# Kernel tuning notes

Measured on AMD Instinct MI355X. Metric: run time of the kernel, lower is better.

Reference implementation:

```python
import jax, jax.numpy as jnp
import numpy as np

N = 50000      # total nodes across batch of graphs
E = 800000     # total directed edges (avg degree 16)
B = 64         # number of graphs
D = 128        # input_dim == hidden_dim
L = 4          # num_layers - 1 GIN layers
OUT = 10
BN_EPS = 1e-5


def setup_inputs() -> dict:
    key = jax.random.key(0)
    ks = jax.random.split(key, 12)
    s = 0.05
    return {
        "x": jax.random.normal(ks[0], (N, D), jnp.float32),
        "pi": jax.random.uniform(ks[1], (B, 25), jnp.float32),
        "eps": jnp.zeros((L,), jnp.float32),
        "mlp_w1": jax.random.normal(ks[2], (L, D, D), jnp.float32) * s,
        "mlp_b1": jnp.zeros((L, D), jnp.float32),
        "mlp_bn_g": jnp.ones((L, D), jnp.float32),
        "mlp_bn_b": jnp.zeros((L, D), jnp.float32),
        "mlp_w2": jax.random.normal(ks[3], (L, D, D), jnp.float32) * s,
        "mlp_b2": jnp.zeros((L, D), jnp.float32),
        "bn_g": jnp.ones((L, D), jnp.float32),
        "bn_b": jnp.zeros((L, D), jnp.float32),
        "attend_w": jax.random.normal(ks[4], (D * (L + 1), 1), jnp.float32) * s,
        "attend_b": jnp.zeros((1,), jnp.float32),
        "pi_w": jax.random.normal(ks[5], (25, 16), jnp.float32) * s,
        "pi_b": jnp.zeros((16,), jnp.float32),
        "out_w": jax.random.normal(ks[6], (D * (L + 1) + 16, OUT), jnp.float32) * s,
        "out_b": jnp.zeros((OUT,), jnp.float32),
        "edge_index": jax.random.randint(ks[7], (2, E), 0, N, dtype=jnp.int32),
        "graph_id": jnp.sort(jax.random.randint(ks[8], (N,), 0, B, dtype=jnp.int32)),
    }


def _bn(z, g, b):
    # BatchNorm1d in training mode over all nodes (axis 0)
    m = z.mean(axis=0)
    v = z.var(axis=0)
    return (z - m) * jax.lax.rsqrt(v + BN_EPS) * g + b


def reference(x, pi, eps, mlp_w1, mlp_b1, mlp_bn_g, mlp_bn_b, mlp_w2, mlp_b2,
              bn_g, bn_b, attend_w, attend_b, pi_w, pi_b, out_w, out_b,
              edge_index, graph_id):
    src, dst = edge_index[0], edge_index[1]
    h = x
    reps = [x]
    for l in range(L):
        # GIN sum aggregation (learn_eps=True: no self-loops in Adj)
        pooled = jax.ops.segment_sum(h[src], dst, num_segments=N)
        pooled = pooled + (1.0 + eps[l]) * h
        # 2-layer MLP: Linear -> BN -> ReLU -> Linear
        z = jax.nn.relu(_bn(pooled @ mlp_w1[l] + mlp_b1[l], mlp_bn_g[l], mlp_bn_b[l]))
        z = z @ mlp_w2[l] + mlp_b2[l]
        # outer BN + ReLU
        h = jax.nn.relu(_bn(z, bn_g[l], bn_b[l]))
        reps.append(h)
    hr = jnp.concatenate(reps, axis=1)               # [N, D*(L+1)]
    # per-graph attention softmax over nodes
    scores = (hr @ attend_w + attend_b)[:, 0]        # [N]
    smax = jax.ops.segment_max(scores, graph_id, num_segments=B)
    e = jnp.exp(scores - smax[graph_id])
    denom = jax.ops.segment_sum(e, graph_id, num_segments=B)
    coef = e / denom[graph_id]
    gemb = jax.ops.segment_sum(hr * coef[:, None], graph_id, num_segments=B)  # [B, D*(L+1)]
    # persistence-image branch (PI computed host-side; treated as input)
    pie = jax.nn.relu(pi @ pi_w + pi_b)              # [B, 16]
    feat = jnp.concatenate([gemb, pie], axis=1)      # [B, D*(L+1)+16]
    return feat @ out_w + out_b                      # [B, OUT]
```

## Files before the change

### kernel.cpp

```cpp
#include <hip/hip_runtime.h>
#include <hip/hip_bf16.h>

#define NN 50000
#define EE 800000
#define BBG 64
#define DD 128
#define LLAY 4
#define HRW 640
#define NOUT 10
#define SCANB 196

typedef __hip_bfloat16 bf16;
typedef __attribute__((ext_vector_type(8))) short short8;
typedef __attribute__((ext_vector_type(4))) float f32x4;

__device__ __forceinline__ float b2f(bf16 v) { return __bfloat162float(v); }
__device__ __forceinline__ float bflo(unsigned u) { return __uint_as_float(u << 16); }
__device__ __forceinline__ float bfhi(unsigned u) { return __uint_as_float(u & 0xffff0000u); }
__device__ __forceinline__ unsigned short f2bs(float v) {
  bf16 h = __float2bfloat16(v);
  unsigned short r; __builtin_memcpy(&r, &h, 2); return r;
}
__device__ __forceinline__ int dtype_of(const void* __restrict__ bng) {
  return (*(const unsigned*)bng == 0x3F800000u) ? 1 : 0;
}
__device__ __forceinline__ float ldf(const void* __restrict__ p, long i, int dt) {
  return dt ? ((const float*)p)[i] : b2f(((const bf16*)p)[i]);
}

__device__ __forceinline__ int lower_bound_i(const int* __restrict__ a, int n, int key) {
  int lo = 0, hi = n;
  while (lo < hi) { int mid = (lo + hi) >> 1; if (a[mid] < key) lo = mid + 1; else hi = mid; }
  return lo;
}

__global__ __launch_bounds__(256) void gnn_init(const void* __restrict__ x,
                                                bf16* __restrict__ hrb,
                                                const void* __restrict__ w1,
                                                const void* __restrict__ w2,
                                                bf16* __restrict__ w1t,
                                                bf16* __restrict__ w2t,
                                                const void* __restrict__ aw,
                                                float* __restrict__ scores,
                                                const int* __restrict__ ei,
                                                int* __restrict__ counts,
                                                int* __restrict__ rel,
                                                const void* __restrict__ bng) {
  int dt = dtype_of(bng);
  int tid = threadIdx.x;
  if (blockIdx.x >= 6250) {
    int i = (blockIdx.x - 6250) * 256 + tid;
    int l = i >> 14, rem = i & 16383, n = rem >> 7, k = rem & 127;
    long src = (long)l * 16384 + k * 128 + n;
    w1t[i] = __float2bfloat16(ldf(w1, src, dt));
    w2t[i] = __float2bfloat16(ldf(w2, src, dt));
    return;
  }
  if (blockIdx.x >= 3125) {
    int e = (blockIdx.x - 3125) * 256 + tid;
    rel[e] = atomicAdd(&counts[ei[EE + e]], 1);
    return;
  }
  int n = blockIdx.x * 16 + (tid >> 4);
  int il = tid & 15;
  long base = (long)n * DD + il * 8;
  float v[8];
  if (dt) {
    float4 a0 = *(const float4*)((const float*)x + base);
    float4 a1 = *(const float4*)((const float*)x + base + 4);
    v[0] = a0.x; v[1] = a0.y; v[2] = a0.z; v[3] = a0.w;
    v[4] = a1.x; v[5] = a1.y; v[6] = a1.z; v[7] = a1.w;
  } else {
    uint4 u = *(const uint4*)((const bf16*)x + base);
    v[0] = bflo(u.x); v[1] = bfhi(u.x); v[2] = bflo(u.y); v[3] = bfhi(u.y);
    v[4] = bflo(u.z); v[5] = bfhi(u.z); v[6] = bflo(u.w); v[7] = bfhi(u.w);
  }
  uint4 o;
  o.x = (unsigned)f2bs(v[0]) | ((unsigned)f2bs(v[1]) << 16);
  o.y = (unsigned)f2bs(v[2]) | ((unsigned)f2bs(v[3]) << 16);
  o.z = (unsigned)f2bs(v[4]) | ((unsigned)f2bs(v[5]) << 16);
  o.w = (unsigned)f2bs(v[6]) | ((unsigned)f2bs(v[7]) << 16);
  *(uint4*)(hrb + (size_t)n * HRW + il * 8) = o;
  float ss = 0.f;
  #pragma unroll
  for (int k = 0; k < 8; k++) ss += v[k] * ldf(aw, il * 8 + k, dt);
  ss += __shfl_xor(ss, 1, 64); ss += __shfl_xor(ss, 2, 64);
  ss += __shfl_xor(ss, 4, 64); ss += __shfl_xor(ss, 8, 64);
  if (il == 0) unsafeAtomicAdd(&scores[n], ss);
}

__global__ __launch_bounds__(256) void gnn_scan1(const int* __restrict__ counts,
                                                 int* __restrict__ blocksum) {
  __shared__ int buf[256];
  int tid = threadIdx.x;
  int i = blockIdx.x * 256 + tid;
  buf[tid] = (i < NN) ? counts[i] : 0;
  __syncthreads();
  for (int s = 128; s > 0; s >>= 1) {
    if (tid < s) buf[tid] += buf[tid + s];
    __syncthreads();
  }
  if (tid == 0) blocksum[blockIdx.x] = buf[0];
}

__global__ __launch_bounds__(256) void gnn_scan3(const int* __restrict__ counts,
                                                 const int* __restrict__ blocksum,
                                                 int* __restrict__ rowstart) {
  __shared__ int buf[256];
  int tid = threadIdx.x;
  int partial = 0;
  for (int i = tid; i < blockIdx.x; i += 256) partial += blocksum[i];
  buf[tid] = partial;
  __syncthreads();
  for (int s = 128; s > 0; s >>= 1) {
    if (tid < s) buf[tid] += buf[tid + s];
    __syncthreads();
  }
  int offset = buf[0];
  __syncthreads();
  int i = blockIdx.x * 256 + tid;
  int v = (i < NN) ? counts[i] : 0;
  buf[tid] = v;
  __syncthreads();
  for (int ofs = 1; ofs < 256; ofs <<= 1) {
    int t = (tid >= ofs) ? buf[tid - ofs] : 0;
    __syncthreads();
    buf[tid] += t;
    __syncthreads();
  }
  int val = offset + buf[tid] - v;
  if (i < NN) rowstart[i] = val;
  if (blockIdx.x == SCANB - 1 && tid == 255) rowstart[NN] = offset + buf[255];
}

__global__ __launch_bounds__(256) void gnn_fill(const int* __restrict__ ei,
                                                const int* __restrict__ rowstart,
                                                const int* __restrict__ rel,
                                                int* __restrict__ csr_src) {
  int e = blockIdx.x * 256 + threadIdx.x;
  int src = ei[e];
  int dst = ei[EE + e];
  csr_src[rowstart[dst] + rel[e]] = src;
}

__device__ __forceinline__ void acc8(float* a, uint4 u) {
  a[0] += bflo(u.x); a[1] += bfhi(u.x);
  a[2] += bflo(u.y); a[3] += bfhi(u.y);
  a[4] += bflo(u.z); a[5] += bfhi(u.z);
  a[6] += bflo(u.w); a[7] += bfhi(u.w);
}

__device__ __forceinline__ float2 statsum(const float* __restrict__ stat, int c) {
  float s = 0.f, q = 0.f;
  #pragma unroll
  for (int k = 0; k < 8; k++) { s += stat[k * 256 + c]; q += stat[k * 256 + 128 + c]; }
  return make_float2(s, q);
}

__global__ __launch_bounds__(512) void gnn_gmg1(const bf16* __restrict__ hrb, int l,
                                                const int* __restrict__ rowstart,
                                                const int* __restrict__ csr_src,
                                                const void* __restrict__ eps,
                                                const bf16* __restrict__ Wt,
                                                const void* __restrict__ bias, int biasOfs,
                                                bf16* __restrict__ out,
                                                float* __restrict__ statOut,
                                                const void* __restrict__ bng) {
  int dt = dtype_of(bng);
  __shared__ __align__(16) unsigned ar[16][68];
  __shared__ int qhead;
  int tid = threadIdx.x, lane = tid & 63;
  int w = tid >> 6;
  int q = lane >> 4, il = lane & 15;
  int r0 = blockIdx.x * 16;
  const bf16* stripe = hrb + l * DD;
  float s = 1.0f + ldf(eps, l, dt);
  if (tid == 0) qhead = 0;
  __syncthreads();

  for (;;) {
    int i;
    if (lane == 0) i = atomicAdd(&qhead, 1);
    i = __shfl(i, 0, 64);
    if (i >= 16) break;
    int n = r0 + i;
    float a[8] = {0.f, 0.f, 0.f, 0.f, 0.f, 0.f, 0.f, 0.f};
    if (q == 0) {
      uint4 u = *(const uint4*)(stripe + (size_t)n * HRW + il * 8);
      a[0] = s * bflo(u.x); a[1] = s * bfhi(u.x);
      a[2] = s * bflo(u.y); a[3] = s * bfhi(u.y);
      a[4] = s * bflo(u.z); a[5] = s * bfhi(u.z);
      a[6] = s * bflo(u.w); a[7] = s * bfhi(u.w);
    }
    int start = rowstart[n], end = rowstart[n + 1];
    for (int base = start; base < end; base += 64) {
      int m = end - base; if (m > 64) m = 64;
      int idx = (base + lane < end) ? csr_src[base + lane] : 0;
      int j = 0;
      for (; j + 16 <= m; j += 16) {
        int s0 = __shfl(idx, j + q, 64);
        int s1 = __shfl(idx, j + 4 + q, 64);
        int s2 = __shfl(idx, j + 8 + q, 64);
        int s3 = __shfl(idx, j + 12 + q, 64);
        uint4 u0 = *(const uint4*)(stripe + (size_t)s0 * HRW + il * 8);
        uint4 u1 = *(const uint4*)(stripe + (size_t)s1 * HRW + il * 8);
        uint4 u2 = *(const uint4*)(stripe + (size_t)s2 * HRW + il * 8);
        uint4 u3 = *(const uint4*)(stripe + (size_t)s3 * HRW + il * 8);
        acc8(a, u0); acc8(a, u1); acc8(a, u2); acc8(a, u3);
      }
      for (; j + 8 <= m; j += 8) {
        int s0 = __shfl(idx, j + q, 64);
        int s1 = __shfl(idx, j + 4 + q, 64);
        uint4 u0 = *(const uint4*)(stripe + (size_t)s0 * HRW + il * 8);
        uint4 u1 = *(const uint4*)(stripe + (size_t)s1 * HRW + il * 8);
        acc8(a, u0); acc8(a, u1);
      }
      for (; j + 4 <= m; j += 4) {
        int src = __shfl(idx, j + q, 64);
        uint4 u = *(const uint4*)(stripe + (size_t)src * HRW + il * 8);
        acc8(a, u);
      }
      for (; j < m; j++) {
        int src = __shfl(idx, j, 64);
        if (q == 0) {
          uint4 u = *(const uint4*)(stripe + (size_t)src * HRW + il * 8);
          acc8(a, u);
        }
      }
    }
    #pragma unroll
    for (int k = 0; k < 8; k++) {
      a[k] += __shfl_xor(a[k], 16, 64);
      a[k] += __shfl_xor(a[k], 32, 64);
    }
    if (q == 0) {
      uint4 o;
      o.x = (unsigned)f2bs(a[0]) | ((unsigned)f2bs(a[1]) << 16);
      o.y = (unsigned)f2bs(a[2]) | ((unsigned)f2bs(a[3]) << 16);
      o.z = (unsigned)f2bs(a[4]) | ((unsigned)f2bs(a[5]) << 16);
      o.w = (unsigned)f2bs(a[6]) | ((unsigned)f2bs(a[7]) << 16);
      *(uint4*)&ar[i][il * 4] = o;
    }
  }
  __syncthreads();

  f32x4 acc = (f32x4){0.f, 0.f, 0.f, 0.f};
  #pragma unroll
  for (int ch = 0; ch < 4; ch++) {
    int k0 = ch * 32 + q * 8;
    uint4 raw = *(const uint4*)&ar[il][ch * 16 + q * 4];
    short8 af;
    __builtin_memcpy(&af, &raw, 16);
    short8 bfv = *(const short8*)(Wt + (w * 16 + il) * DD + k0);
    acc = __builtin_amdgcn_mfma_f32_16x16x32_bf16(af, bfv, acc, 0, 0, 0);
  }
  int col = w * 16 + il;
  float bv = ldf(bias, biasOfs + col, dt);
  float ss = 0.f, qq = 0.f;
  #pragma unroll
  for (int r = 0; r < 4; r++) {
    int row = r0 + q * 4 + r;
    float v = acc[r] + bv;
    out[(size_t)row * DD + col] = __float2bfloat16(v);
    ss += v; qq += v * v;
  }
  ss += __shfl_xor(ss, 16, 64);  ss += __shfl_xor(ss, 32, 64);
  qq += __shfl_xor(qq, 16, 64);  qq += __shfl_xor(qq, 32, 64);
  if (q == 0) {
    unsafeAtomicAdd(&statOut[(blockIdx.x & 7) * 256 + col], ss);
    unsafeAtomicAdd(&statOut[(blockIdx.x & 7) * 256 + 128 + col], qq);
  }
}

__global__ __launch_bounds__(256) void gnn_mgemm(const bf16* __restrict__ Abf,
                                                 const bf16* __restrict__ Wt,
                                                 const void* __restrict__ bias, int biasOfs,
                                                 bf16* __restrict__ out,
                                                 const float* __restrict__ statIn,
                                                 const void* __restrict__ g,
                                                 const void* __restrict__ bb, int parOfs,
                                                 float* __restrict__ statOut,
                                                 const void* __restrict__ bng) {
  int dt = dtype_of(bng);
  __shared__ float scf[128], shf[128];
  __shared__ float redS[4][128], redQ[4][128];
  int tid = threadIdx.x, w = tid >> 6, lane = tid & 63;
  int q = lane >> 4, il = lane & 15;
  if (tid < 128) {
    const float invN = 1.0f / NN;
    float2 sq = statsum(statIn, tid);
    float m = sq.x * invN;
    float rs = rsqrtf(sq.y * invN - m * m + 1e-5f);
    float gg = ldf(g, parOfs + tid, dt), bv = ldf(bb, parOfs + tid, dt);
    scf[tid] = rs * gg;
    shf[tid] = bv - m * rs * gg;
  }
  __syncthreads();
  int r0 = (blockIdx.x * 4 + w) * 16;
  int arow = r0 + il;
  int arowc = (arow < NN) ? arow : (NN - 1);
  f32x4 acc[8];
  #pragma unroll
  for (int i = 0; i < 8; i++) acc[i] = (f32x4){0.f, 0.f, 0.f, 0.f};
  #pragma unroll
  for (int ch = 0; ch < 4; ch++) {
    int k0 = ch * 32 + q * 8;
    uint4 raw = *(const uint4*)(Abf + (size_t)arowc * DD + k0);
    float4 c0 = *(const float4*)(scf + k0);
    float4 c1 = *(const float4*)(scf + k0 + 4);
    float4 d0 = *(const float4*)(shf + k0);
    float4 d1 = *(const float4*)(shf + k0 + 4);
    short8 af;
    af[0] = (short)f2bs(fmaxf(bflo(raw.x) * c0.x + d0.x, 0.f));
    af[1] = (short)f2bs(fmaxf(bfhi(raw.x) * c0.y + d0.y, 0.f));
    af[2] = (short)f2bs(fmaxf(bflo(raw.y) * c0.z + d0.z, 0.f));
    af[3] = (short)f2bs(fmaxf(bfhi(raw.y) * c0.w + d0.w, 0.f));
    af[4] = (short)f2bs(fmaxf(bflo(raw.z) * c1.x + d1.x, 0.f));
    af[5] = (short)f2bs(fmaxf(bfhi(raw.z) * c1.y + d1.y, 0.f));
    af[6] = (short)f2bs(fmaxf(bflo(raw.w) * c1.z + d1.z, 0.f));
    af[7] = (short)f2bs(fmaxf(bfhi(raw.w) * c1.w + d1.w, 0.f));
    #pragma unroll
    for (int ct = 0; ct < 8; ct++) {
      short8 bfv = *(const short8*)(Wt + (ct * 16 + il) * DD + k0);
      acc[ct] = __builtin_amdgcn_mfma_f32_16x16x32_bf16(af, bfv, acc[ct], 0, 0, 0);
    }
  }
  #pragma unroll
  for (int ct = 0; ct < 8; ct++) {
    int col = ct * 16 + il;
    float bv = ldf(bias, biasOfs + col, dt);
    float s = 0.f, qq = 0.f;
    #pragma unroll
    for (int r = 0; r < 4; r++) {
      int row = r0 + q * 4 + r;
      float v = acc[ct][r] + bv;
      if (row < NN) {
        out[(size_t)row * DD + col] = __float2bfloat16(v);
        s += v; qq += v * v;
      }
    }
    s += __shfl_xor(s, 16, 64);  s += __shfl_xor(s, 32, 64);
    qq += __shfl_xor(qq, 16, 64); qq += __shfl_xor(qq, 32, 64);
    if (q == 0) { redS[w][col] = s; redQ[w][col] = qq; }
  }
  __syncthreads();
  if (tid < 128) {
    float v = redS[0][tid] + redS[1][tid] + redS[2][tid] + redS[3][tid];
    unsafeAtomicAdd(&statOut[(blockIdx.x & 7) * 256 + tid], v);
  } else {
    int c = tid - 128;
    float v = redQ[0][c] + redQ[1][c] + redQ[2][c] + redQ[3][c];
    unsafeAtomicAdd(&statOut[(blockIdx.x & 7) * 256 + 128 + c], v);
  }
}

__global__ __launch_bounds__(256) void gnn_bn_relu(const bf16* __restrict__ z2,
                                                   const float* __restrict__ stat,
                                                   const void* __restrict__ g,
                                                   const void* __restrict__ bb, int parOfs,
                                                   bf16* __restrict__ hrb, int stripe,
                                                   const void* __restrict__ aw,
                                                   float* __restrict__ scores,
                                                   const void* __restrict__ bng) {
  int dt = dtype_of(bng);
  __shared__ float scf[128], shf[128], awf[128];
  int tid = threadIdx.x;
  if (tid < 128) {
    const float invN = 1.0f / NN;
    float2 sq = statsum(stat, tid);
    float m = sq.x * invN;
    float rs = rsqrtf(sq.y * invN - m * m + 1e-5f);
    float gg = ldf(g, parOfs + tid, dt), bv = ldf(bb, parOfs + tid, dt);
    scf[tid] = rs * gg;
    shf[tid] = bv - m * rs * gg;
    awf[tid] = ldf(aw, stripe * DD + tid, dt);
  }
  __syncthreads();
  int n = blockIdx.x * 16 + (tid >> 4);
  int il = tid & 15;
  int c0 = il * 8;
  uint4 u = *(const uint4*)(z2 + (size_t)n * DD + c0);
  float v[8];
  v[0] = bflo(u.x); v[1] = bfhi(u.x); v[2] = bflo(u.y); v[3] = bfhi(u.y);
  v[4] = bflo(u.z); v[5] = bfhi(u.z); v[6] = bflo(u.w); v[7] = bfhi(u.w);
  float ss = 0.f;
  #pragma unroll
  for (int k = 0; k < 8; k++) {
    v[k] = fmaxf(v[k] * scf[c0 + k] + shf[c0 + k], 0.f);
    ss += v[k] * awf[c0 + k];
  }
  uint4 o;
  o.x = (unsigned)f2bs(v[0]) | ((unsigned)f2bs(v[1]) << 16);
  o.y = (unsigned)f2bs(v[2]) | ((unsigned)f2bs(v[3]) << 16);
  o.z = (unsigned)f2bs(v[4]) | ((unsigned)f2bs(v[5]) << 16);
  o.w = (unsigned)f2bs(v[6]) | ((unsigned)f2bs(v[7]) << 16);
  *(uint4*)(hrb + (size_t)n * HRW + stripe * DD + c0) = o;
  ss += __shfl_xor(ss, 1, 64); ss += __shfl_xor(ss, 2, 64);
  ss += __shfl_xor(ss, 4, 64); ss += __shfl_xor(ss, 8, 64);
  if (il == 0) unsafeAtomicAdd(&scores[n], ss);
}

__global__ __launch_bounds__(128) void gnn_gemb(const bf16* __restrict__ hrb,
                                                const float* __restrict__ scores,
                                                const int* __restrict__ gid,
                                                float* __restrict__ gemb) {
  int b = blockIdx.x / 40;
  int part = blockIdx.x % 40;
  int chunk = part % 5;
  int slice = part / 5;
  int tid = threadIdx.x;
  int start = lower_bound_i(gid, NN, b);
  int end = lower_bound_i(gid, NN, b + 1);
  __shared__ float red[128];
  float mx = -3.4e38f;
  for (int n = start + tid; n < end; n += 128) mx = fmaxf(mx, scores[n]);
  red[tid] = mx;
  __syncthreads();
  for (int s = 64; s > 0; s >>= 1) {
    if (tid < s) red[tid] = fmaxf(red[tid], red[tid + s]);
    __syncthreads();
  }
  float smax = red[0];
  __syncthreads();
  float sum = 0.f;
  for (int n = start + tid; n < end; n += 128) sum += __expf(scores[n] - smax);
  red[tid] = sum;
  __syncthreads();
  for (int s = 64; s > 0; s >>= 1) {
    if (tid < s) red[tid] += red[tid + s];
    __syncthreads();
  }
  float denom = red[0];
  float inv = (denom > 0.f) ? 1.0f / denom : 0.f;
  int c = chunk * 128 + tid;
  float acc = 0.f;
  for (int n = start + slice; n < end; n += 8)
    acc += b2f(hrb[(size_t)n * HRW + c]) * __expf(scores[n] - smax) * inv;
  unsafeAtomicAdd(&gemb[b * HRW + c], acc);
}

__global__ __launch_bounds__(64) void gnn_final(const float* __restrict__ gemb,
                                                const void* __restrict__ pi,
                                                const void* __restrict__ piw,
                                                const void* __restrict__ pib,
                                                const void* __restrict__ ow,
                                                const void* __restrict__ ob,
                                                void* __restrict__ out,
                                                const void* __restrict__ bng) {
  int dt = dtype_of(bng);
  int b = blockIdx.x;
  int t = threadIdx.x;
  __shared__ float pie[16];
  if (t < 16) {
    float s = ldf(pib, t, dt);
    for (int i = 0; i < 25; i++) s += ldf(pi, b * 25 + i, dt) * ldf(piw, i * 16 + t, dt);
    pie[t] = fmaxf(s, 0.f);
  }
  __syncthreads();
  for (int o = 0; o < NOUT; o++) {
    float s = 0.f;
    for (int c = t; c < HRW + 16; c += 64) {
      float f = (c < HRW) ? gemb[b * HRW + c] : pie[c - HRW];
      s += f * ldf(ow, c * NOUT + o, dt);
    }
    #pragma unroll
    for (int m = 32; m > 0; m >>= 1) s += __shfl_xor(s, m, 64);
    if (t == 0) {
      float r = s + ldf(ob, o, dt);
      if (dt) ((float*)out)[b * NOUT + o] = r;
      else ((bf16*)out)[b * NOUT + o] = __float2bfloat16(r);
    }
  }
}

extern "C" void kernel_launch(void* const* d_in, const int* in_sizes, int n_in,
                              void* d_out, int out_size, void* d_ws, size_t ws_size,
                              hipStream_t stream) {
  const void* x    = d_in[0];
  const void* pi   = d_in[1];
  const void* eps  = d_in[2];
  const void* w1   = d_in[3];
  const void* b1   = d_in[4];
  const void* bng  = d_in[5];
  const void* bnb  = d_in[6];
  const void* w2   = d_in[7];
  const void* b2   = d_in[8];
  const void* obng = d_in[9];
  const void* obnb = d_in[10];
  const void* aw   = d_in[11];
  const void* piw  = d_in[13];
  const void* pib  = d_in[14];
  const void* ow   = d_in[15];
  const void* ob   = d_in[16];
  const int*  ei   = (const int*)d_in[17];
  const int*  gid  = (const int*)d_in[18];

  bf16*  hrb      = (bf16*)d_ws;
  bf16*  z1       = hrb + (size_t)NN * HRW;
  bf16*  z2       = z1 + (size_t)NN * DD;
  bf16*  w1t      = z2 + (size_t)NN * DD;
  bf16*  w2t      = w1t + LLAY * DD * DD;
  float* statbufs = (float*)(w2t + LLAY * DD * DD);
  float* gemb     = statbufs + 8 * 2048;
  int*   counts   = (int*)(gemb + BBG * HRW);
  float* scores   = (float*)(counts + NN);
  size_t zeroBytes = (size_t)(8 * 2048 + BBG * HRW + NN + NN) * 4;
  int*   rowstart = (int*)(scores + NN);
  int*   rel      = rowstart + NN + 1;
  int*   csr_src  = rel + EE;
  int*   blocksum = csr_src + EE;

  hipMemsetAsync(statbufs, 0, zeroBytes, stream);
  gnn_init<<<6506, 256, 0, stream>>>(x, hrb, w1, w2, w1t, w2t, aw, scores,
                                     ei, counts, rel, bng);

  gnn_scan1<<<SCANB, 256, 0, stream>>>(counts, blocksum);
  gnn_scan3<<<SCANB, 256, 0, stream>>>(counts, blocksum, rowstart);
  gnn_fill<<<EE / 256, 256, 0, stream>>>(ei, rowstart, rel, csr_src);

  for (int l = 0; l < LLAY; l++) {
    float* statA = statbufs + (l * 2 + 0) * 2048;
    float* statB = statbufs + (l * 2 + 1) * 2048;
    gnn_gmg1<<<NN / 16, 512, 0, stream>>>(hrb, l, rowstart, csr_src, eps,
                                          w1t + l * DD * DD, b1, l * DD,
                                          z1, statA, bng);
    gnn_mgemm<<<782, 256, 0, stream>>>(z1, w2t + l * DD * DD, b2, l * DD,
                                       z2, statA, bng, bnb, l * DD,
                                       statB, bng);
    gnn_bn_relu<<<NN / 16, 256, 0, stream>>>(z2, statB, obng, obnb, l * DD,
                                             hrb, l + 1, aw, scores, bng);
  }

  gnn_gemb<<<BBG * 40, 128, 0, stream>>>(hrb, scores, gid, gemb);
  gnn_final<<<BBG, 64, 0, stream>>>(gemb, pi, piw, pib, ow, ob, d_out, bng);
}
```

Baseline: 554.7 us.

## Fuse outer BN+ReLU of previous layer into next layer's gather-GEMM kernel

```diff
diff --git a/kernel.cpp b/kernel.cpp
--- a/kernel.cpp
+++ b/kernel.cpp
@@ -86,7 +86,7 @@
   for (int k = 0; k < 8; k++) ss += v[k] * ldf(aw, il * 8 + k, dt);
   ss += __shfl_xor(ss, 1, 64); ss += __shfl_xor(ss, 2, 64);
   ss += __shfl_xor(ss, 4, 64); ss += __shfl_xor(ss, 8, 64);
-  if (il == 0) unsafeAtomicAdd(&scores[n], ss);
+  if (il == 0) scores[n] = ss;
 }
 
 __global__ __launch_bounds__(256) void gnn_scan1(const int* __restrict__ counts,
@@ -149,6 +149,17 @@
   a[4] += bflo(u.z); a[5] += bfhi(u.z);
   a[6] += bflo(u.w); a[7] += bfhi(u.w);
 }
+__device__ __forceinline__ void acc8bn(float* a, uint4 u,
+                                       const float* sc, const float* sh) {
+  a[0] += fmaxf(fmaf(bflo(u.x), sc[0], sh[0]), 0.f);
+  a[1] += fmaxf(fmaf(bfhi(u.x), sc[1], sh[1]), 0.f);
+  a[2] += fmaxf(fmaf(bflo(u.y), sc[2], sh[2]), 0.f);
+  a[3] += fmaxf(fmaf(bfhi(u.y), sc[3], sh[3]), 0.f);
+  a[4] += fmaxf(fmaf(bflo(u.z), sc[4], sh[4]), 0.f);
+  a[5] += fmaxf(fmaf(bfhi(u.z), sc[5], sh[5]), 0.f);
+  a[6] += fmaxf(fmaf(bflo(u.w), sc[6], sh[6]), 0.f);
+  a[7] += fmaxf(fmaf(bfhi(u.w), sc[7], sh[7]), 0.f);
+}
 
 __device__ __forceinline__ float2 statsum(const float* __restrict__ stat, int c) {
   float s = 0.f, q = 0.f;
@@ -157,10 +168,17 @@
   return make_float2(s, q);
 }
 
-__global__ __launch_bounds__(512) void gnn_gmg1(const bf16* __restrict__ hrb, int l,
+template<int BN>
+__global__ __launch_bounds__(512) void gnn_gmg1(const bf16* __restrict__ src, int srcPitch,
+                                                const float* __restrict__ statIn,
+                                                const void* __restrict__ g,
+                                                const void* __restrict__ bb, int parOfs,
+                                                bf16* __restrict__ hrbOut,
+                                                const void* __restrict__ aw, int awOfs,
+                                                float* __restrict__ scores,
                                                 const int* __restrict__ rowstart,
                                                 const int* __restrict__ csr_src,
-                                                const void* __restrict__ eps,
+                                                const void* __restrict__ eps, int l,
                                                 const bf16* __restrict__ Wt,
                                                 const void* __restrict__ bias, int biasOfs,
                                                 bf16* __restrict__ out,
@@ -169,14 +187,31 @@
   int dt = dtype_of(bng);
   __shared__ __align__(16) unsigned ar[16][68];
   __shared__ int qhead;
+  __shared__ float scfS[128], shfS[128], awfS[128];
   int tid = threadIdx.x, lane = tid & 63;
   int w = tid >> 6;
   int q = lane >> 4, il = lane & 15;
   int r0 = blockIdx.x * 16;
-  const bf16* stripe = hrb + l * DD;
+  if (BN && tid < 128) {
+    const float invN = 1.0f / NN;
+    float2 sq = statsum(statIn, tid);
+    float m = sq.x * invN;
+    float rs = rsqrtf(sq.y * invN - m * m + 1e-5f);
+    float gg = ldf(g, parOfs + tid, dt), bv = ldf(bb, parOfs + tid, dt);
+    scfS[tid] = rs * gg;
+    shfS[tid] = bv - m * rs * gg;
+    awfS[tid] = ldf(aw, awOfs + tid, dt);
+  }
+  if (tid == 0) qhead = 0;
+  __syncthreads();
+  float sc[8], sh[8], af8[8];
+  if (BN) {
+    #pragma unroll
+    for (int k = 0; k < 8; k++) {
+      sc[k] = scfS[il * 8 + k]; sh[k] = shfS[il * 8 + k]; af8[k] = awfS[il * 8 + k];
+    }
+  }
   float s = 1.0f + ldf(eps, l, dt);
-  if (tid == 0) qhead = 0;
-  __syncthreads();
 
   for (;;) {
     int i;
@@ -186,11 +221,28 @@
     int n = r0 + i;
     float a[8] = {0.f, 0.f, 0.f, 0.f, 0.f, 0.f, 0.f, 0.f};
     if (q == 0) {
-      uint4 u = *(const uint4*)(stripe + (size_t)n * HRW + il * 8);
-      a[0] = s * bflo(u.x); a[1] = s * bfhi(u.x);
-      a[2] = s * bflo(u.y); a[3] = s * bfhi(u.y);
-      a[4] = s * bflo(u.z); a[5] = s * bfhi(u.z);
-      a[6] = s * bflo(u.w); a[7] = s * bfhi(u.w);
+      uint4 u = *(const uint4*)(src + (size_t)n * srcPitch + il * 8);
+      float v[8];
+      v[0] = bflo(u.x); v[1] = bfhi(u.x); v[2] = bflo(u.y); v[3] = bfhi(u.y);
+      v[4] = bflo(u.z); v[5] = bfhi(u.z); v[6] = bflo(u.w); v[7] = bfhi(u.w);
+      if (BN) {
+        #pragma unroll
+        for (int k = 0; k < 8; k++) v[k] = fmaxf(fmaf(v[k], sc[k], sh[k]), 0.f);
+        uint4 o;
+        o.x = (unsigned)f2bs(v[0]) | ((unsigned)f2bs(v[1]) << 16);
+        o.y = (unsigned)f2bs(v[2]) | ((unsigned)f2bs(v[3]) << 16);
+        o.z = (unsigned)f2bs(v[4]) | ((unsigned)f2bs(v[5]) << 16);
+        o.w = (unsigned)f2bs(v[6]) | ((unsigned)f2bs(v[7]) << 16);
+        *(uint4*)(hrbOut + (size_t)n * HRW + il * 8) = o;
+        float sscore = 0.f;
+        #pragma unroll
+        for (int k = 0; k < 8; k++) sscore += v[k] * af8[k];
+        sscore += __shfl_xor(sscore, 1, 64); sscore += __shfl_xor(sscore, 2, 64);
+        sscore += __shfl_xor(sscore, 4, 64); sscore += __shfl_xor(sscore, 8, 64);
+        if (il == 0) scores[n] += sscore;
+      }
+      #pragma unroll
+      for (int k = 0; k < 8; k++) a[k] = s * v[k];
     }
     int start = rowstart[n], end = rowstart[n + 1];
     for (int base = start; base < end; base += 64) {
@@ -202,29 +254,32 @@
         int s1 = __shfl(idx, j + 4 + q, 64);
         int s2 = __shfl(idx, j + 8 + q, 64);
         int s3 = __shfl(idx, j + 12 + q, 64);
-        uint4 u0 = *(const uint4*)(stripe + (size_t)s0 * HRW + il * 8);
-        uint4 u1 = *(const uint4*)(stripe + (size_t)s1 * HRW + il * 8);
-        uint4 u2 = *(const uint4*)(stripe + (size_t)s2 * HRW + il * 8);
-        uint4 u3 = *(const uint4*)(stripe + (size_t)s3 * HRW + il * 8);
-        acc8(a, u0); acc8(a, u1); acc8(a, u2); acc8(a, u3);
+        uint4 u0 = *(const uint4*)(src + (size_t)s0 * srcPitch + il * 8);
+        uint4 u1 = *(const uint4*)(src + (size_t)s1 * srcPitch + il * 8);
+        uint4 u2 = *(const uint4*)(src + (size_t)s2 * srcPitch + il * 8);
+        uint4 u3 = *(const uint4*)(src + (size_t)s3 * srcPitch + il * 8);
+        if (BN) { acc8bn(a, u0, sc, sh); acc8bn(a, u1, sc, sh);
+                  acc8bn(a, u2, sc, sh); acc8bn(a, u3, sc, sh); }
+        else    { acc8(a, u0); acc8(a, u1); acc8(a, u2); acc8(a, u3); }
       }
       for (; j + 8 <= m; j += 8) {
         int s0 = __shfl(idx, j + q, 64);
         int s1 = __shfl(idx, j + 4 + q, 64);
-        uint4 u0 = *(const uint4*)(stripe + (size_t)s0 * HRW + il * 8);
-        uint4 u1 = *(const uint4*)(stripe + (size_t)s1 * HRW + il * 8);
-        acc8(a, u0); acc8(a, u1);
+        uint4 u0 = *(const uint4*)(src + (size_t)s0 * srcPitch + il * 8);
+        uint4 u1 = *(const uint4*)(src + (size_t)s1 * srcPitch + il * 8);
+        if (BN) { acc8bn(a, u0, sc, sh); acc8bn(a, u1, sc, sh); }
+        else    { acc8(a, u0); acc8(a, u1); }
       }
       for (; j + 4 <= m; j += 4) {
-        int src = __shfl(idx, j + q, 64);
-        uint4 u = *(const uint4*)(stripe + (size_t)src * HRW + il * 8);
-        acc8(a, u);
+        int s0 = __shfl(idx, j + q, 64);
+        uint4 u = *(const uint4*)(src + (size_t)s0 * srcPitch + il * 8);
+        if (BN) acc8bn(a, u, sc, sh); else acc8(a, u);
       }
       for (; j < m; j++) {
-        int src = __shfl(idx, j, 64);
+        int s0 = __shfl(idx, j, 64);
         if (q == 0) {
-          uint4 u = *(const uint4*)(stripe + (size_t)src * HRW + il * 8);
-          acc8(a, u);
+          uint4 u = *(const uint4*)(src + (size_t)s0 * srcPitch + il * 8);
+          if (BN) acc8bn(a, u, sc, sh); else acc8(a, u);
         }
       }
     }
@@ -397,7 +452,7 @@
   *(uint4*)(hrb + (size_t)n * HRW + stripe * DD + c0) = o;
   ss += __shfl_xor(ss, 1, 64); ss += __shfl_xor(ss, 2, 64);
   ss += __shfl_xor(ss, 4, 64); ss += __shfl_xor(ss, 8, 64);
-  if (il == 0) unsafeAtomicAdd(&scores[n], ss);
+  if (il == 0) scores[n] += ss;
 }
 
 __global__ __launch_bounds__(128) void gnn_gemb(const bf16* __restrict__ hrb,
@@ -521,16 +576,29 @@
   for (int l = 0; l < LLAY; l++) {
     float* statA = statbufs + (l * 2 + 0) * 2048;
     float* statB = statbufs + (l * 2 + 1) * 2048;
-    gnn_gmg1<<<NN / 16, 512, 0, stream>>>(hrb, l, rowstart, csr_src, eps,
-                                          w1t + l * DD * DD, b1, l * DD,
-                                          z1, statA, bng);
+    if (l == 0) {
+      gnn_gmg1<0><<<NN / 16, 512, 0, stream>>>(hrb, HRW,
+                                               nullptr, nullptr, nullptr, 0,
+                                               nullptr, nullptr, 0, nullptr,
+                                               rowstart, csr_src, eps, 0,
+                                               w1t, b1, 0, z1, statA, bng);
+    } else {
+      float* statPrev = statbufs + ((l - 1) * 2 + 1) * 2048;
+      gnn_gmg1<1><<<NN / 16, 512, 0, stream>>>(z2, DD,
+                                               statPrev, obng, obnb, (l - 1) * DD,
+                                               hrb + l * DD, aw, l * DD, scores,
+                                               rowstart, csr_src, eps, l,
+                                               w1t + l * DD * DD, b1, l * DD,
+                                               z1, statA, bng);
+    }
     gnn_mgemm<<<782, 256, 0, stream>>>(z1, w2t + l * DD * DD, b2, l * DD,
                                        z2, statA, bng, bnb, l * DD,
                                        statB, bng);
-    gnn_bn_relu<<<NN / 16, 256, 0, stream>>>(z2, statB, obng, obnb, l * DD,
-                                             hrb, l + 1, aw, scores, bng);
-  }
-
+  }
+
+  gnn_bn_relu<<<NN / 16, 256, 0, stream>>>(z2, statbufs + 7 * 2048,
+                                           obng, obnb, 3 * DD,
+                                           hrb, 4, aw, scores, bng);
   gnn_gemb<<<BBG * 40, 128, 0, stream>>>(hrb, scores, gid, gemb);
   gnn_final<<<BBG, 64, 0, stream>>>(gemb, pi, piw, pib, ow, ob, d_out, bng);
 }
```

New measurement: 637.8 us. 1.15x slower.
